# Kernel optimization log

Hardware: AMD Instinct MI355X
Metric: run time of the kernel (lower is better)

## Reference

```python
import jax, jax.numpy as jnp
import numpy as np
import math

NUM_USER, NUM_COURSE, NUM_TEACHER, NUM_SCHOOL = 100000, 10000, 5000, 3000
D = 16
B, LS, LT, LSC = 1024, 200, 10, 5
NC, LU, LS2, LT2 = 100, 50, 3, 5


def setup_inputs() -> dict:
    key = jax.random.key(0)
    ks = jax.random.split(key, 32)
    sig = 1.0 / D  # torch init: normal(0, 1/num_dim) on ALL params (overwrites padding row too)
    p = lambda k, shp: jax.random.normal(k, shp, jnp.float32) * sig
    ri = lambda k, shp, hi: jax.random.randint(k, shp, 0, hi)
    inp = {}
    inp['user_idx']       = ri(ks[0], (B, 1), NUM_USER)
    inp['user_sequence']  = ri(ks[1], (B, LS), NUM_COURSE + 1)   # may hit padding idx
    inp['user_teachers']  = ri(ks[2], (B, LT), NUM_TEACHER + 1)
    inp['user_school']    = ri(ks[3], (B, LSC), NUM_SCHOOL + 1)
    inp['user_len_seq']     = jax.random.randint(ks[4], (B, 1), 1, LS + 1).astype(jnp.float32)
    inp['user_len_teacher'] = jax.random.randint(ks[5], (B, 1), 1, LT + 1).astype(jnp.float32)
    inp['user_len_school']  = jax.random.randint(ks[6], (B, 1), 1, LSC + 1).astype(jnp.float32)
    inp['course_set']     = ri(ks[7], (B, NC), NUM_COURSE)
    inp['course_user']    = ri(ks[8], (B, NC, LU), NUM_USER + 1)
    inp['course_school']  = ri(ks[9], (B, NC, LS2), NUM_SCHOOL + 1)
    inp['course_teacher'] = ri(ks[10], (B, NC, LT2), NUM_TEACHER + 1)
    inp['course_len_u']       = jax.random.randint(ks[11], (B, NC), 1, LU + 1).astype(jnp.float32)
    inp['course_len_teacher'] = jax.random.randint(ks[12], (B, NC), 1, LT2 + 1).astype(jnp.float32)
    # learned parameters (jax layout: Linear weight is [in, out])
    inp['user_table']    = p(ks[13], (NUM_USER + 1, D))
    inp['course_table']  = p(ks[14], (NUM_COURSE + 1, D))
    inp['teacher_table'] = p(ks[15], (NUM_TEACHER + 1, D))
    inp['school_table']  = p(ks[16], (NUM_SCHOOL + 1, D))
    inp['Qw'] = p(ks[17], (D, D)); inp['Qb'] = p(ks[18], (D,))
    inp['Kw'] = p(ks[19], (D, D)); inp['Kb'] = p(ks[20], (D,))
    inp['g1w'] = p(ks[21], (2 * D, D)); inp['g1b'] = p(ks[22], (D,))
    inp['g2w'] = p(ks[23], (D, D));     inp['g2b'] = p(ks[24], (D,))
    inp['caw1'] = p(ks[25], (D, D)); inp['cab1'] = p(ks[26], (D,))
    inp['caw2'] = p(ks[27], (D, 1))
    return inp


def _transformer(x, Qw, Qb, Kw, Kb):
    # x: [B, L, d] -> [B, d]. Faithful to source: K is RESHAPED (not transposed) to [B, d, L].
    b, L, d = x.shape
    Q = jax.nn.relu(x @ Qw + Qb)                       # [B, L, d]
    K = jax.nn.relu(x @ Kw + Kb).reshape(b, d, L)      # reshape, as in source
    s = jnp.matmul(Q, K) / math.sqrt(d)                # [B, L, L]
    s = jnp.where(jnp.eye(L, dtype=bool), jnp.float32(1e-32), s)  # diag set to 1e-32
    su = jax.nn.softmax(s, axis=2)
    a = jnp.matmul(su, x)                              # [B, L, d]
    return a.mean(axis=1)


def reference(user_idx, user_sequence, user_teachers, user_school,
              user_len_seq, user_len_teacher, user_len_school,
              course_set, course_user, course_school, course_teacher,
              course_len_u, course_len_teacher,
              user_table, course_table, teacher_table, school_table,
              Qw, Qb, Kw, Kb, g1w, g1b, g2w, g2b, caw1, cab1, caw2):
    # ---- user side ----
    user_emb = user_table[user_idx[:, 0]]                       # [B, d]
    seq_emb = course_table[user_sequence]                       # [B, LS, d]
    seq_rep = _transformer(seq_emb, Qw, Qb, Kw, Kb)             # [B, d]
    ut_mean = teacher_table[user_teachers].sum(axis=1) / user_len_teacher
    us_mean = school_table[user_school].sum(axis=1) / user_len_school
    agg = (seq_rep + ut_mean + us_mean) / 3.0
    h = jnp.concatenate([user_emb, agg], axis=1)                # [B, 2d]
    user_final = jax.nn.relu(h @ g1w + g1b) @ g2w + g2b         # [B, d]
    # ---- course side ----
    course_emb = course_table[course_set]                       # [B, Nc, d]
    cu_mean = user_table[course_user].sum(axis=2) / course_len_u[..., None]
    cs_sum  = school_table[course_school].sum(axis=2)           # note: no division (as in source)
    ct_mean = teacher_table[course_teacher].sum(axis=2) / course_len_teacher[..., None]
    nb = jnp.stack([cu_mean, cs_sum, ct_mean], axis=2)          # [B, Nc, 3, d]
    att = jax.nn.softmax(jax.nn.sigmoid(nb @ caw1 + cab1) @ caw2, axis=2)
    _course_agg = (nb * att).sum(axis=2)  # computed in source but unused (dead code)
    # ---- score ----
    out = jnp.sum(user_final[:, None, :] * course_emb, axis=2)  # [B, Nc]
    return out
```

## Files before the change

kernel.cpp:

```cpp
#include <hip/hip_runtime.h>
#include <hip/hip_bf16.h>

#define NBATCH 1024
#define LSEQ   200
#define DD     16
#define LTT    10
#define LSCH   5
#define NCC    100

#define XT_S   232
#define QB_S   24
#define KT_S   24
#define WT_S   20

#define QSCALE 0.3606737602f

typedef __bf16 bf16_4 __attribute__((ext_vector_type(4)));
typedef float  f32x4  __attribute__((ext_vector_type(4)));
typedef short  short4v __attribute__((ext_vector_type(4)));
typedef unsigned int uint2v __attribute__((ext_vector_type(2)));

__device__ __forceinline__ int kswz(int j) { return ((j >> 3) ^ (j >> 6)) & 1; }

__device__ __forceinline__ f32x4 mfma16(bf16_4 a, bf16_4 b, f32x4 c) {
#if __has_builtin(__builtin_amdgcn_mfma_f32_16x16x16bf16_1k)
    return __builtin_amdgcn_mfma_f32_16x16x16bf16_1k(
        __builtin_bit_cast(short4v, a), __builtin_bit_cast(short4v, b), c, 0, 0, 0);
#else
    uint2v au = __builtin_bit_cast(uint2v, a);
    uint2v bu = __builtin_bit_cast(uint2v, b);
    asm("v_mfma_f32_16x16x16_bf16 %0, %1, %2, %0" : "+v"(c) : "v"(au), "v"(bu));
    return c;
#endif
}

__global__ __launch_bounds__(256, 4) void hin_kernel(
    const int*   __restrict__ user_idx,
    const int*   __restrict__ user_sequence,
    const int*   __restrict__ user_teachers,
    const int*   __restrict__ user_school,
    const float* __restrict__ user_len_teacher,
    const float* __restrict__ user_len_school,
    const int*   __restrict__ course_set,
    const float* __restrict__ user_table,
    const float* __restrict__ course_table,
    const float* __restrict__ teacher_table,
    const float* __restrict__ school_table,
    const float* __restrict__ Qw, const float* __restrict__ Qb,
    const float* __restrict__ Kw, const float* __restrict__ Kb,
    const float* __restrict__ g1w, const float* __restrict__ g1b,
    const float* __restrict__ g2w, const float* __restrict__ g2b,
    float*       __restrict__ out)
{
    __shared__ __align__(16) __bf16 xt[DD * XT_S];
    __shared__ __align__(16) __bf16 qb[208 * QB_S];
    __shared__ __align__(16) __bf16 kt[208 * KT_S];
    __shared__ __align__(16) __bf16 wqt[DD * WT_S], wkt[DD * WT_S];
    __shared__ float bQv[DD], bKv[DD];
    __shared__ float red[4][DD];
    __shared__ float uf[DD];
    __shared__ float gst[800];
    __shared__ float rows_pre[256];
    __shared__ float lens[2];
    __shared__ int   csets[NCC];

    const int b    = blockIdx.x;
    const int t    = threadIdx.x;
    const int w    = t >> 6;
    const int lane = t & 63;
    const int grp  = lane >> 4;
    const int li   = lane & 15;

    {
        const int k = t >> 4, n = t & 15;
        wqt[n*WT_S + k] = (__bf16)Qw[k*DD + n];
        wkt[n*WT_S + k] = (__bf16)Kw[k*DD + n];
    }
    if (t < DD) { bQv[t] = Qb[t]; bKv[t] = Kb[t]; }
    if (t < 128)
        xt[(t >> 3)*XT_S + 200 + (t & 7)] = (__bf16)0.f;
    else {
        const int i = t - 128;
        kt[(200 + (i >> 4))*KT_S + (i & 15)] = (__bf16)0.f;
    }
    for (int i = t; i < 800; i += 256) {
        float v;
        if      (i < 512) v = g1w[i];
        else if (i < 528) v = g1b[i - 512];
        else if (i < 784) v = g2w[i - 528];
        else              v = g2b[i - 784];
        gst[i] = v;
    }
    if (t < 16)       rows_pre[t] = user_table[user_idx[b]*DD + t];
    else if (t < 176) { const int i = t - 16;
        rows_pre[t] = teacher_table[user_teachers[b*LTT + (i >> 4)]*DD + (i & 15)]; }
    else if (t < 256) { const int i = t - 176;
        rows_pre[t] = school_table[user_school[b*LSCH + (i >> 4)]*DD + (i & 15)]; }
    if (t == 0) { lens[0] = user_len_teacher[b]; lens[1] = user_len_school[b]; }
    if (t < NCC) csets[t] = course_set[b*NCC + t];

    for (int e = t; e < 800; e += 256) {
        const int l = e >> 2, dq = e & 3;
        const int idx = user_sequence[b*LSEQ + l];
        const float4 v = *(const float4*)&course_table[idx*DD + dq*4];
        xt[(dq*4+0)*XT_S + l] = (__bf16)v.x;
        xt[(dq*4+1)*XT_S + l] = (__bf16)v.y;
        xt[(dq*4+2)*XT_S + l] = (__bf16)v.z;
        xt[(dq*4+3)*XT_S + l] = (__bf16)v.w;
    }
    __syncthreads();

    {
        float qbias[4];
        #pragma unroll
        for (int r = 0; r < 4; r++) qbias[r] = bQv[grp*4 + r];
        const float kbias = bKv[li];
        const bf16_4 wq = *(const bf16_4*)&wqt[li*WT_S + grp*4];
        const bf16_4 wk = *(const bf16_4*)&wkt[li*WT_S + grp*4];
        for (int mt = w; mt < 13; mt += 4) {
            const int l0 = mt * 16;
            bf16_4 xf;
            #pragma unroll
            for (int e = 0; e < 4; e++)
                xf[e] = xt[(grp*4 + e)*XT_S + l0 + li];
            const f32x4 zc = {0.f, 0.f, 0.f, 0.f};
            f32x4 qv = mfma16(wq, xf, zc);
            f32x4 kv = mfma16(xf, wk, zc);
            bf16_4 qpk;
            #pragma unroll
            for (int r = 0; r < 4; r++)
                qpk[r] = (__bf16)(QSCALE * fmaxf(qv[r] + qbias[r], 0.f));
            *(bf16_4*)&qb[(l0 + li)*QB_S + grp*4] = qpk;
            #pragma unroll
            for (int r = 0; r < 4; r++) {
                const int lrow = l0 + grp*4 + r;
                if (lrow < LSEQ) {
                    const float val = fmaxf(kv[r] + kbias, 0.f);
                    const int f = lrow*DD + li;
                    const int p = f / 200;
                    const int j = f - p*200;
                    kt[j*KT_S + (p ^ (kswz(j) << 3))] = (__bf16)val;
                }
            }
        }
    }
    __syncthreads();

    float wsum = 0.f;
    const int dr = li - grp*4;

    for (int mt = w; mt < 13; mt += 4) {
        const int m0 = mt * 16;
        const bf16_4 qf = *(const bf16_4*)&qb[(m0 + li)*QB_S + grp*4];

        f32x4 acc0 = {0.f, 0.f, 0.f, 0.f};
        f32x4 acc1 = {0.f, 0.f, 0.f, 0.f};
        f32x4 psv  = {0.f, 0.f, 0.f, 0.f};

        #pragma unroll
        for (int jt = 0; jt < 13; jt++) {
            const int jr = jt*16 + li;
            const bf16_4 kf = *(const bf16_4*)&kt[jr*KT_S + ((grp*4) ^ (kswz(jr) << 3))];
            const f32x4 zc = {0.f, 0.f, 0.f, 0.f};
            f32x4 s = mfma16(kf, qf, zc);
            bf16_4 pa;
            #pragma unroll
            for (int r = 0; r < 4; r++) {
                float pv = __builtin_amdgcn_exp2f(s[r]);
                if (jt == 12 && grp >= 2) pv = 0.f;
                if (jt == mt && dr == r)  pv = 1.0f;
                psv[r] += pv;
                pa[r] = (__bf16)pv;
            }
            const bf16_4 xb = *(const bf16_4*)&xt[li*XT_S + jt*16 + grp*4];
            if (jt & 1) acc1 = mfma16(pa, xb, acc1);
            else        acc0 = mfma16(pa, xb, acc0);
        }

        float tot = (psv[0] + psv[1]) + (psv[2] + psv[3]);
        tot += __shfl_xor(tot, 16);
        tot += __shfl_xor(tot, 32);
        #pragma unroll
        for (int r = 0; r < 4; r++) {
            const int grow = m0 + grp*4 + r;
            const float dsum = __shfl(tot, grp*4 + r);
            const float a = (acc0[r] + acc1[r]) * __builtin_amdgcn_rcpf(dsum);
            wsum += (grow < LSEQ) ? a : 0.f;
        }
    }
    wsum += __shfl_xor(wsum, 16);
    wsum += __shfl_xor(wsum, 32);
    if (lane < DD) red[w][lane] = wsum;
    __syncthreads();

    if (w == 0) {
        const float ue  = rows_pre[li];
        const float seq = (red[0][li] + red[1][li] + red[2][li] + red[3][li]) * (1.0f / LSEQ);
        float uts = 0.f;
        #pragma unroll
        for (int i = 0; i < LTT; i++)  uts += rows_pre[16 + i*16 + li];
        float uss = 0.f;
        #pragma unroll
        for (int i = 0; i < LSCH; i++) uss += rows_pre[176 + i*16 + li];
        const float agg = (seq + uts / lens[0] + uss / lens[1]) * (1.0f / 3.0f);
        float a1 = gst[512 + li];
        #pragma unroll
        for (int k = 0; k < 16; k++) a1 = fmaf(__shfl(ue,  k), gst[k*DD + li], a1);
        #pragma unroll
        for (int k = 0; k < 16; k++) a1 = fmaf(__shfl(agg, k), gst[(16 + k)*DD + li], a1);
        const float hidv = fmaxf(a1, 0.f);
        float a2 = gst[784 + li];
        #pragma unroll
        for (int k = 0; k < 16; k++) a2 = fmaf(__shfl(hidv, k), gst[528 + k*DD + li], a2);
        if (lane < DD) uf[lane] = a2;
    }
    __syncthreads();

    if (t < NCC) {
        const int ci = csets[t];
        const float* ce = &course_table[ci*DD];
        float s = 0.f;
        #pragma unroll
        for (int g = 0; g < 4; g++) {
            const float4 cv = *(const float4*)&ce[g*4];
            const float4 uv = *(const float4*)&uf[g*4];
            s += cv.x*uv.x + cv.y*uv.y + cv.z*uv.z + cv.w*uv.w;
        }
        out[b*NCC + t] = s;
    }
}

extern "C" void kernel_launch(void* const* d_in, const int* in_sizes, int n_in,
                              void* d_out, int out_size, void* d_ws, size_t ws_size,
                              hipStream_t stream) {
    const int*   user_idx         = (const int*)  d_in[0];
    const int*   user_sequence    = (const int*)  d_in[1];
    const int*   user_teachers    = (const int*)  d_in[2];
    const int*   user_school      = (const int*)  d_in[3];
    const float* user_len_teacher = (const float*)d_in[5];
    const float* user_len_school  = (const float*)d_in[6];
    const int*   course_set       = (const int*)  d_in[7];
    const float* user_table       = (const float*)d_in[13];
    const float* course_table     = (const float*)d_in[14];
    const float* teacher_table    = (const float*)d_in[15];
    const float* school_table     = (const float*)d_in[16];
    const float* Qw  = (const float*)d_in[17];
    const float* Qb  = (const float*)d_in[18];
    const float* Kw  = (const float*)d_in[19];
    const float* Kb  = (const float*)d_in[20];
    const float* g1w = (const float*)d_in[21];
    const float* g1b = (const float*)d_in[22];
    const float* g2w = (const float*)d_in[23];
    const float* g2b = (const float*)d_in[24];

    float* outp = (float*)d_out;

    hipLaunchKernelGGL(hin_kernel, dim3(NBATCH), dim3(256), 0, stream,
                       user_idx, user_sequence, user_teachers, user_school,
                       user_len_teacher, user_len_school, course_set,
                       user_table, course_table, teacher_table, school_table,
                       Qw, Qb, Kw, Kb, g1w, g1b, g2w, g2b, outp);
}
```

Measured before the change: 23.54 us.

## Split last query tile across waves and cache K/X fragments in registers

Wave 0 used to handle four query tiles while the other waves handled three. The 13th query tile (rows 192-207) is now split across all four waves by key-tile ranges, and partial softmax denominators are combined through shared memory after an extra barrier. K and X fragments are loaded once into registers before the loop, which removes repeated LDS reads. The cost is higher register pressure, an added __syncthreads, and predicated extra MFMA work.

```diff
diff --git a/kernel.cpp b/kernel.cpp
--- a/kernel.cpp
+++ b/kernel.cpp
@@ -58,6 +58,7 @@
     __shared__ __align__(16) __bf16 wqt[DD * WT_S], wkt[DD * WT_S];
     __shared__ float bQv[DD], bKv[DD];
     __shared__ float red[4][DD];
+    __shared__ __align__(16) float tot12t[64];
     __shared__ float uf[DD];
     __shared__ float gst[800];
     __shared__ float rows_pre[256];
@@ -146,10 +147,22 @@
     }
     __syncthreads();
 
+    const int wu = __builtin_amdgcn_readfirstlane(w);
+    const int dr = li - grp*4;
+
+    bf16_4 kfr[13], xbr[13];
+    #pragma unroll
+    for (int jt = 0; jt < 13; jt++) {
+        const int jr = jt*16 + li;
+        kfr[jt] = *(const bf16_4*)&kt[jr*KT_S + ((grp*4) ^ (kswz(jr) << 3))];
+        xbr[jt] = *(const bf16_4*)&xt[li*XT_S + jt*16 + grp*4];
+    }
+
     float wsum = 0.f;
-    const int dr = li - grp*4;
-
-    for (int mt = w; mt < 13; mt += 4) {
+
+    #pragma unroll
+    for (int mi = 0; mi < 3; mi++) {
+        const int mt = wu + mi*4;
         const int m0 = mt * 16;
         const bf16_4 qf = *(const bf16_4*)&qb[(m0 + li)*QB_S + grp*4];
 
@@ -159,10 +172,8 @@
 
         #pragma unroll
         for (int jt = 0; jt < 13; jt++) {
-            const int jr = jt*16 + li;
-            const bf16_4 kf = *(const bf16_4*)&kt[jr*KT_S + ((grp*4) ^ (kswz(jr) << 3))];
             const f32x4 zc = {0.f, 0.f, 0.f, 0.f};
-            f32x4 s = mfma16(kf, qf, zc);
+            f32x4 s = mfma16(kfr[jt], qf, zc);
             bf16_4 pa;
             #pragma unroll
             for (int r = 0; r < 4; r++) {
@@ -172,9 +183,8 @@
                 psv[r] += pv;
                 pa[r] = (__bf16)pv;
             }
-            const bf16_4 xb = *(const bf16_4*)&xt[li*XT_S + jt*16 + grp*4];
-            if (jt & 1) acc1 = mfma16(pa, xb, acc1);
-            else        acc0 = mfma16(pa, xb, acc0);
+            if (jt & 1) acc1 = mfma16(pa, xbr[jt], acc1);
+            else        acc0 = mfma16(pa, xbr[jt], acc0);
         }
 
         float tot = (psv[0] + psv[1]) + (psv[2] + psv[3]);
@@ -182,12 +192,50 @@
         tot += __shfl_xor(tot, 32);
         #pragma unroll
         for (int r = 0; r < 4; r++) {
-            const int grow = m0 + grp*4 + r;
             const float dsum = __shfl(tot, grp*4 + r);
-            const float a = (acc0[r] + acc1[r]) * __builtin_amdgcn_rcpf(dsum);
-            wsum += (grow < LSEQ) ? a : 0.f;
-        }
-    }
+            wsum += (acc0[r] + acc1[r]) * __builtin_amdgcn_rcpf(dsum);
+        }
+    }
+
+    f32x4 acc12 = {0.f, 0.f, 0.f, 0.f};
+    {
+        const int jlo = (wu == 0) ? 0 : (3*wu + 1);
+        const int jhi = 3*wu + 4;
+        const bf16_4 qf = *(const bf16_4*)&qb[(192 + li)*QB_S + grp*4];
+        f32x4 psv = {0.f, 0.f, 0.f, 0.f};
+        #pragma unroll
+        for (int jt = 0; jt < 13; jt++) {
+            if (jt >= jlo && jt < jhi) {
+                const f32x4 zc = {0.f, 0.f, 0.f, 0.f};
+                f32x4 s = mfma16(kfr[jt], qf, zc);
+                bf16_4 pa;
+                #pragma unroll
+                for (int r = 0; r < 4; r++) {
+                    float pv = __builtin_amdgcn_exp2f(s[r]);
+                    if (jt == 12 && grp >= 2) pv = 0.f;
+                    if (jt == 12 && dr == r)  pv = 1.0f;
+                    psv[r] += pv;
+                    pa[r] = (__bf16)pv;
+                }
+                acc12 = mfma16(pa, xbr[jt], acc12);
+            }
+        }
+        float tot = (psv[0] + psv[1]) + (psv[2] + psv[3]);
+        tot += __shfl_xor(tot, 16);
+        tot += __shfl_xor(tot, 32);
+        if (lane < 16) tot12t[li*4 + w] = tot;
+    }
+    __syncthreads();
+
+    #pragma unroll
+    for (int r = 0; r < 4; r++) {
+        const int q = grp*4 + r;
+        const float4 p4 = *(const float4*)&tot12t[q*4];
+        const float dsum = (p4.x + p4.y) + (p4.z + p4.w);
+        const float a = acc12[r] * __builtin_amdgcn_rcpf(dsum);
+        wsum += (192 + q < LSEQ) ? a : 0.f;
+    }
+
     wsum += __shfl_xor(wsum, 16);
     wsum += __shfl_xor(wsum, 32);
     if (lane < DD) red[w][lane] = wsum;
```

Measured after the change: 21.71 us. 7.8% less time.
